# Optimization experiments

Measured on AMD Instinct MI355X. Metric: run time of the kernel, lower is better.

The kernel has to match this reference:

```python
import jax, jax.numpy as jnp
import numpy as np

L, B, T, V, E, H = 6, 4, 1024, 32000, 768, 12
D = E // H  # head_size = 64


def setup_inputs() -> dict:
    key = jax.random.key(0)
    ks = jax.random.split(key, 12)
    s = 0.02
    n = lambda k, shape: jax.random.normal(k, shape, jnp.float32) * s
    return {
        "idx": jax.random.randint(ks[0], (B, T), 0, V),
        "tok_emb": n(ks[1], (V, E)),
        "pos_emb": n(ks[2], (T, E)),
        "ln1_w": jnp.ones((L, E)), "ln1_b": jnp.zeros((L, E)),
        "wq": n(ks[3], (L, E, H, D)),
        "wk": n(ks[4], (L, E, H, D)),
        "wv": n(ks[5], (L, E, H, D)),
        "wo": n(ks[6], (L, E, E)), "bo": jnp.zeros((L, E)),
        "ln2_w": jnp.ones((L, E)), "ln2_b": jnp.zeros((L, E)),
        "w1": n(ks[7], (L, E, 4 * E)), "b1": jnp.zeros((L, 4 * E)),
        "w2": n(ks[8], (L, 4 * E, E)), "b2": jnp.zeros((L, E)),
        "lnf_w": jnp.ones((E,)), "lnf_b": jnp.zeros((E,)),
        "head_w": n(ks[9], (E, V)), "head_b": jnp.zeros((V,)),
    }


def _ln(x, w, b, eps=1e-5):
    m = x.mean(-1, keepdims=True)
    v = ((x - m) ** 2).mean(-1, keepdims=True)
    return (x - m) * jax.lax.rsqrt(v + eps) * w + b


def _forward(idx, tok_emb, pos_emb, ln1_w, ln1_b, wq, wk, wv, wo, bo,
             ln2_w, ln2_b, w1, b1, w2, b2, lnf_w, lnf_b, head_w, head_b):
    t = idx.shape[1]
    x = tok_emb[idx] + pos_emb[None, :t]          # [B,T,E]
    causal = jnp.tril(jnp.ones((t, t), bool))     # tril buffer
    scale = jnp.asarray(D, x.dtype) ** -0.5       # k.shape[-1] ** -0.5

    def block(x, p):
        l1w, l1b, Wq, Wk, Wv, Wo, Bo, l2w, l2b, W1, B1, W2, B2 = p
        h = _ln(x, l1w, l1b)
        q = jnp.einsum('btc,chd->bthd', h, Wq)
        k = jnp.einsum('btc,chd->bthd', h, Wk)
        v = jnp.einsum('btc,chd->bthd', h, Wv)
        wei = jnp.einsum('bqhd,bkhd->bhqk', q, k) * scale
        wei = jnp.where(causal, wei, -jnp.inf)
        wei = jax.nn.softmax(wei, axis=-1)
        att = jnp.einsum('bhqk,bkhd->bqhd', wei, v).reshape(x.shape)
        x = x + (att @ Wo + Bo)
        h2 = _ln(x, l2w, l2b)
        x = x + (jax.nn.relu(h2 @ W1 + B1) @ W2 + B2)
        return x, None

    params = (ln1_w, ln1_b, wq, wk, wv, wo, bo, ln2_w, ln2_b, w1, b1, w2, b2)
    x, _ = jax.lax.scan(block, x, params)
    x = _ln(x, lnf_w, lnf_b)
    return x @ head_w + head_b                    # [B,T,V] logits


def reference(idx, tok_emb, pos_emb, ln1_w, ln1_b, wq, wk, wv, wo, bo,
              ln2_w, ln2_b, w1, b1, w2, b2, lnf_w, lnf_b, head_w, head_b):
    return _forward(idx, tok_emb, pos_emb, ln1_w, ln1_b, wq, wk, wv, wo, bo,
                    ln2_w, ln2_b, w1, b1, w2, b2, lnf_w, lnf_b, head_w, head_b)
```

## Files before the change

### kernel.cpp

```cpp
#include <hip/hip_runtime.h>
#include <hip/hip_bf16.h>
#include <math.h>

#define L_LAYERS 6
#define BB 4
#define TT 1024
#define VV 32000
#define EE 768
#define HH 12
#define DD 64
#define BT (BB * TT)

typedef unsigned short u16;
typedef unsigned int   u32;
typedef __attribute__((ext_vector_type(8))) short short8;
typedef __attribute__((ext_vector_type(8))) unsigned short ushort8v;
typedef __attribute__((ext_vector_type(4))) float f32x4;

__device__ __forceinline__ float b2f_lo(u32 u) { union { u32 i; float f; } c; c.i = u << 16;          return c.f; }
__device__ __forceinline__ float b2f_hi(u32 u) { union { u32 i; float f; } c; c.i = u & 0xffff0000u;  return c.f; }
__device__ __forceinline__ u16  f2b(float f)   { union { float f; u32 i; } c{f}; u32 r = c.i + 0x7fffu + ((c.i >> 16) & 1u); return (u16)(r >> 16); }

__device__ __forceinline__ void gload16(const void* g, void* l) {
    __builtin_amdgcn_global_load_lds(
        (const __attribute__((address_space(1))) void*)g,
        (__attribute__((address_space(3))) void*)l, 16, 0, 0);
}

__global__ __launch_bounds__(256) void embed_kernel(
    const int* __restrict__ idx, const float* __restrict__ tok_emb,
    const float* __restrict__ pos_emb, float* __restrict__ x)
{
    int i = blockIdx.x * 256 + threadIdx.x;
    int e  = i % EE;
    int bt = i / EE;
    int t  = bt % TT;
    int tok = idx[bt];
    x[i] = tok_emb[(size_t)tok * EE + e] + pos_emb[(size_t)t * EE + e];
}

__global__ __launch_bounds__(256) void ln_kernel(
    const float* __restrict__ X, const float* __restrict__ w,
    const float* __restrict__ b, u16* __restrict__ Y)
{
    const int tid = threadIdx.x;
    const size_t row = blockIdx.x;
    const float* x = X + row * EE;

    float v0 = x[tid], v1 = x[tid + 256], v2 = x[tid + 512];

    __shared__ float red[256];
    red[tid] = v0 + v1 + v2;
    __syncthreads();
    for (int off = 128; off > 0; off >>= 1) {
        if (tid < off) red[tid] += red[tid + off];
        __syncthreads();
    }
    float mean = red[0] * (1.0f / EE);
    __syncthreads();
    float d0 = v0 - mean, d1 = v1 - mean, d2 = v2 - mean;
    red[tid] = d0 * d0 + d1 * d1 + d2 * d2;
    __syncthreads();
    for (int off = 128; off > 0; off >>= 1) {
        if (tid < off) red[tid] += red[tid + off];
        __syncthreads();
    }
    float rstd = rsqrtf(red[0] * (1.0f / EE) + 1e-5f);

    u16* y = Y + row * EE;
    y[tid]       = f2b(d0 * rstd * w[tid]       + b[tid]);
    y[tid + 256] = f2b(d1 * rstd * w[tid + 256] + b[tid + 256]);
    y[tid + 512] = f2b(d2 * rstd * w[tid + 512] + b[tid + 512]);
}

__device__ __forceinline__ void transpose_tile(
    const float* __restrict__ W, u16* __restrict__ Wt,
    int K, int N, int kt, int nt)
{
    __shared__ float t[32][33];
    const int k0 = kt * 32;
    const int n0 = nt * 32;
    const int c = threadIdx.x & 31;
    const int r = threadIdx.x >> 5;
    #pragma unroll
    for (int i = 0; i < 4; i++)
        t[r + i * 8][c] = W[(size_t)(k0 + r + i * 8) * N + n0 + c];
    __syncthreads();
    #pragma unroll
    for (int i = 0; i < 4; i++) {
        int rr = r + i * 8;
        Wt[(size_t)(n0 + rr) * K + k0 + c] = f2b(t[c][rr]);
    }
}

__global__ __launch_bounds__(256) void transpose_cvt(
    const float* __restrict__ W, u16* __restrict__ Wt, int K, int N)
{
    transpose_tile(W, Wt, K, N, blockIdx.y, blockIdx.x);
}

__global__ __launch_bounds__(256) void transpose_layer(
    const float* __restrict__ wq, const float* __restrict__ wk,
    const float* __restrict__ wv, const float* __restrict__ wo,
    const float* __restrict__ w1, const float* __restrict__ w2,
    u16* __restrict__ wt)
{
    const int t = blockIdx.x;
    if (t < 2304) {
        const int m = t / 576, r = t % 576;
        const float* Ws[4] = {wq, wk, wv, wo};
        transpose_tile(Ws[m], wt + (size_t)m * 768 * 768, 768, 768, r / 24, r % 24);
    } else if (t < 4608) {
        const int r = t - 2304;
        transpose_tile(w1, wt + (size_t)4 * 768 * 768, 768, 3072, r / 96, r % 96);
    } else {
        const int r = t - 4608;
        transpose_tile(w2, wt + (size_t)4 * 768 * 768 + (size_t)3072 * 768,
                       3072, 768, r / 24, r % 24);
    }
}

template<int RELU, int RES, int OUTBF, int MFRAG>
__global__ __launch_bounds__(256) void gemm_bf16(
    const u16* __restrict__ A, const u16* __restrict__ Bt,
    const float* __restrict__ bias, const float* __restrict__ res,
    void* __restrict__ Cv, int M, int N, int K)
{
    constexpr int TM = MFRAG * 32;
    __shared__ u16 As[TM * 64];
    __shared__ u16 Bs[128 * 64];

    const int tid  = threadIdx.x;
    const int lane = tid & 63;
    const int w    = tid >> 6;
    const int wr   = w >> 1, wc = w & 1;
    const int m0 = blockIdx.x * TM;
    const int n0 = blockIdx.y * 128;

    const int cs = (lane & 7) ^ (lane >> 3);
    const int rl = lane >> 3;

    int aoff[2 * MFRAG], boff[8];
    const int kq = lane >> 4;
    #pragma unroll
    for (int mi = 0; mi < MFRAG; mi++) {
        int rg = wr * (MFRAG * 16) + mi * 16 + (lane & 15);
        #pragma unroll
        for (int ks = 0; ks < 2; ks++)
            aoff[2 * mi + ks] = rg * 64 + (((ks * 4 + kq) ^ (rg & 7)) * 8);
    }
    #pragma unroll
    for (int ni = 0; ni < 4; ni++) {
        int rg = wc * 64 + ni * 16 + (lane & 15);
        #pragma unroll
        for (int ks = 0; ks < 2; ks++)
            boff[2 * ni + ks] = rg * 64 + (((ks * 4 + kq) ^ (rg & 7)) * 8);
    }

    f32x4 acc[MFRAG][4] = {};

    for (int k0 = 0; k0 < K; k0 += 64) {
        __syncthreads();
        #pragma unroll
        for (int i = 0; i < MFRAG; i++) {
            const int seg = i * 4 + w;
            const int row = seg * 8 + rl;
            gload16(A + (size_t)(m0 + row) * K + k0 + cs * 8, &As[seg * 512]);
        }
        #pragma unroll
        for (int i = 0; i < 4; i++) {
            const int seg = i * 4 + w;
            const int row = seg * 8 + rl;
            gload16(Bt + (size_t)(n0 + row) * K + k0 + cs * 8, &Bs[seg * 512]);
        }
        __syncthreads();
        #pragma unroll
        for (int ks = 0; ks < 2; ks++) {
            short8 af[MFRAG], bfv[4];
            #pragma unroll
            for (int mi = 0; mi < MFRAG; mi++) af[mi] = *(const short8*)&As[aoff[2 * mi + ks]];
            #pragma unroll
            for (int ni = 0; ni < 4; ni++) bfv[ni] = *(const short8*)&Bs[boff[2 * ni + ks]];
            #pragma unroll
            for (int mi = 0; mi < MFRAG; mi++)
                #pragma unroll
                for (int ni = 0; ni < 4; ni++)
                    acc[mi][ni] = __builtin_amdgcn_mfma_f32_16x16x32_bf16(
                        af[mi], bfv[ni], acc[mi][ni], 0, 0, 0);
        }
    }

    const int rbase = m0 + wr * (MFRAG * 16) + (lane >> 4) * 4;
    const int cbase = n0 + wc * 64 + (lane & 15);
    #pragma unroll
    for (int ni = 0; ni < 4; ni++) {
        const int c = cbase + ni * 16;
        const float bv = bias ? bias[c] : 0.0f;
        #pragma unroll
        for (int mi = 0; mi < MFRAG; mi++) {
            const int r = rbase + mi * 16;
            #pragma unroll
            for (int i = 0; i < 4; i++) {
                float v = acc[mi][ni][i] + bv;
                const size_t off = (size_t)(r + i) * N + c;
                if (RES)  v += res[off];
                if (RELU) v = fmaxf(v, 0.0f);
                if (OUTBF) ((u16*)Cv)[off] = f2b(v);
                else       ((float*)Cv)[off] = v;
            }
        }
    }
}

template<int RELU, int OUTBF>
__global__ __launch_bounds__(512, 2) void gemm256(
    const u16* __restrict__ A, const u16* __restrict__ Bt,
    const float* __restrict__ bias, void* __restrict__ Cv,
    int M, int N, int K)
{
    __shared__ u16 SA[2][256 * 64];
    __shared__ u16 SB[2][256 * 64];

    const int tid  = threadIdx.x;
    const int lane = tid & 63;
    const int w    = tid >> 6;
    const int wr   = w >> 2, wc = w & 3;

    const int gx  = gridDim.x;
    const int nwg = gx * gridDim.y;
    const int lin = blockIdx.y * gx + blockIdx.x;
    const int q8  = nwg >> 3;
    const int s   = (lin & 7) * q8 + (lin >> 3);
    const int m0  = (s % gx) * 256;
    const int n0  = (s / gx) * 256;

    const int cs = (lane & 7) ^ (lane >> 3);
    const int rl = lane >> 3;

    const int lr = lane & 15, kq = lane >> 4;
    int aoff[16], boff[8];
    #pragma unroll
    for (int mi = 0; mi < 8; mi++) {
        int rg = wr * 128 + mi * 16 + lr;
        #pragma unroll
        for (int ks = 0; ks < 2; ks++)
            aoff[2 * mi + ks] = rg * 64 + (((ks * 4 + kq) ^ (rg & 7)) * 8);
    }
    #pragma unroll
    for (int ni = 0; ni < 4; ni++) {
        int rg = wc * 64 + ni * 16 + lr;
        #pragma unroll
        for (int ks = 0; ks < 2; ks++)
            boff[2 * ni + ks] = rg * 64 + (((ks * 4 + kq) ^ (rg & 7)) * 8);
    }

    const int nt = K >> 6;

    auto STAGE = [&](int t, int bf) {
        const int k0 = t * 64;
        #pragma unroll
        for (int i = 0; i < 4; i++) {
            const int seg = i * 8 + w;
            const int row = seg * 8 + rl;
            gload16(A + (size_t)(m0 + row) * K + k0 + cs * 8, &SA[bf][seg * 512]);
        }
        #pragma unroll
        for (int i = 0; i < 4; i++) {
            const int seg = i * 8 + w;
            const int row = seg * 8 + rl;
            gload16(Bt + (size_t)(n0 + row) * K + k0 + cs * 8, &SB[bf][seg * 512]);
        }
    };

    f32x4 acc[8][4] = {};

    STAGE(0, 0);
    STAGE(1, 1);
    asm volatile("s_waitcnt vmcnt(8)" ::: "memory");
    __builtin_amdgcn_s_barrier();
    __builtin_amdgcn_sched_barrier(0);

    for (int t = 0; t < nt; t++) {
        const int cur = t & 1;
        __builtin_amdgcn_s_setprio(1);
        #pragma unroll
        for (int ks = 0; ks < 2; ks++) {
            short8 af[8], bv[4];
            #pragma unroll
            for (int mi = 0; mi < 8; mi++) af[mi] = *(const short8*)&SA[cur][aoff[2 * mi + ks]];
            #pragma unroll
            for (int ni = 0; ni < 4; ni++) bv[ni] = *(const short8*)&SB[cur][boff[2 * ni + ks]];
            #pragma unroll
            for (int mi = 0; mi < 8; mi++)
                #pragma unroll
                for (int ni = 0; ni < 4; ni++)
                    acc[mi][ni] = __builtin_amdgcn_mfma_f32_16x16x32_bf16(
                        af[mi], bv[ni], acc[mi][ni], 0, 0, 0);
        }
        __builtin_amdgcn_s_setprio(0);

        if (t < nt - 1) {
            __builtin_amdgcn_sched_barrier(0);
            __builtin_amdgcn_s_barrier();
            __builtin_amdgcn_sched_barrier(0);
            if (t + 2 < nt) {
                STAGE(t + 2, cur);
                asm volatile("s_waitcnt vmcnt(8)" ::: "memory");
            } else {
                asm volatile("s_waitcnt vmcnt(0)" ::: "memory");
            }
            __builtin_amdgcn_sched_barrier(0);
            __builtin_amdgcn_s_barrier();
            __builtin_amdgcn_sched_barrier(0);
        }
    }

    const int rbase = m0 + wr * 128 + (lane >> 4) * 4;
    const int cbase = n0 + wc * 64 + lr;
    #pragma unroll
    for (int ni = 0; ni < 4; ni++) {
        const int c = cbase + ni * 16;
        const float bvf = bias ? bias[c] : 0.0f;
        #pragma unroll
        for (int mi = 0; mi < 8; mi++) {
            const int r = rbase + mi * 16;
            #pragma unroll
            for (int i = 0; i < 4; i++) {
                float v = acc[mi][ni][i] + bvf;
                if (RELU) v = fmaxf(v, 0.0f);
                const size_t off = (size_t)(r + i) * N + c;
                if (OUTBF) ((u16*)Cv)[off] = f2b(v);
                else       ((float*)Cv)[off] = v;
            }
        }
    }
}

#define AST 76
__global__ __launch_bounds__(256) void attn_mfma(
    const u16* __restrict__ qkv, u16* __restrict__ O)
{
    const int tid = threadIdx.x;
    const int qi = blockIdx.x;
    const int h  = blockIdx.y;
    const int b  = blockIdx.z;
    const int q0 = qi * 64;

    __shared__ u16 Ks[64 * AST];
    __shared__ u16 Vt[64 * AST];
    __shared__ u16 Ps[64 * AST];

    const int lane = tid & 63;
    const int w    = tid >> 6;
    const int lr   = lane & 15;
    const int lk   = lane >> 4;

    const int sr = tid >> 2;
    const int sc = tid & 3;

    {
        const u16* src = qkv + (size_t)(b * TT + q0 + sr) * 2304 + h * 64 + sc * 16;
        *(ushort8v*)&Ps[sr * AST + sc * 16]     = *(const ushort8v*)src;
        *(ushort8v*)&Ps[sr * AST + sc * 16 + 8] = *(const ushort8v*)(src + 8);
    }
    __syncthreads();
    short8 aq[2];
    #pragma unroll
    for (int ks = 0; ks < 2; ks++)
        aq[ks] = *(const short8*)&Ps[(w * 16 + lr) * AST + lk * 8 + ks * 32];

    f32x4 oacc[4] = {};
    float m_run[4], l_run[4];
    #pragma unroll
    for (int i = 0; i < 4; i++) { m_run[i] = -3.0e38f; l_run[i] = 0.0f; }

    const int qrow = q0 + w * 16 + lk * 4;
    const int ntile = qi + 1;

    for (int t = 0; t < ntile; t++) {
        const int k0 = t * 64;
        __syncthreads();
        {
            const u16* ksrc = qkv + (size_t)(b * TT + k0 + sr) * 2304 + 768 + h * 64 + sc * 16;
            *(ushort8v*)&Ks[sr * AST + sc * 16]     = *(const ushort8v*)ksrc;
            *(ushort8v*)&Ks[sr * AST + sc * 16 + 8] = *(const ushort8v*)(ksrc + 8);
            const u16* vsrc = ksrc + 768;
            ushort8v v0 = *(const ushort8v*)vsrc;
            ushort8v v1 = *(const ushort8v*)(vsrc + 8);
            #pragma unroll
            for (int j = 0; j < 8; j++) Vt[(sc * 16 + j) * AST + sr]     = v0[j];
            #pragma unroll
            for (int j = 0; j < 8; j++) Vt[(sc * 16 + 8 + j) * AST + sr] = v1[j];
        }
        __syncthreads();

        f32x4 sfrag[4] = {};
        #pragma unroll
        for (int ks = 0; ks < 2; ks++)
            #pragma unroll
            for (int nt = 0; nt < 4; nt++) {
                short8 bk = *(const short8*)&Ks[(nt * 16 + lr) * AST + lk * 8 + ks * 32];
                sfrag[nt] = __builtin_amdgcn_mfma_f32_16x16x32_bf16(aq[ks], bk, sfrag[nt], 0, 0, 0);
            }

        float sv[4][4];
        #pragma unroll
        for (int i = 0; i < 4; i++) {
            float mx = -3.0e38f;
            #pragma unroll
            for (int nt = 0; nt < 4; nt++) {
                float s = sfrag[nt][i] * 0.125f;
                if (t == qi && (k0 + nt * 16 + lr) > (qrow + i)) s = -3.0e38f;
                sv[i][nt] = s;
                mx = fmaxf(mx, s);
            }
            mx = fmaxf(mx, __shfl_xor(mx, 1));
            mx = fmaxf(mx, __shfl_xor(mx, 2));
            mx = fmaxf(mx, __shfl_xor(mx, 4));
            mx = fmaxf(mx, __shfl_xor(mx, 8));
            const float m_new = fmaxf(m_run[i], mx);
            const float scale = __expf(m_run[i] - m_new);
            float rs = 0.0f;
            #pragma unroll
            for (int nt = 0; nt < 4; nt++) {
                float p = __expf(sv[i][nt] - m_new);
                sv[i][nt] = p;
                rs += p;
            }
            rs += __shfl_xor(rs, 1);
            rs += __shfl_xor(rs, 2);
            rs += __shfl_xor(rs, 4);
            rs += __shfl_xor(rs, 8);
            l_run[i] = l_run[i] * scale + rs;
            m_run[i] = m_new;
            #pragma unroll
            for (int dt = 0; dt < 4; dt++) oacc[dt][i] *= scale;
        }

        #pragma unroll
        for (int i = 0; i < 4; i++)
            #pragma unroll
            for (int nt = 0; nt < 4; nt++)
                Ps[(w * 16 + lk * 4 + i) * AST + nt * 16 + lr] = f2b(sv[i][nt]);
        __syncthreads();

        #pragma unroll
        for (int ks = 0; ks < 2; ks++) {
            short8 ap = *(const short8*)&Ps[(w * 16 + lr) * AST + lk * 8 + ks * 32];
            #pragma unroll
            for (int dt = 0; dt < 4; dt++) {
                short8 bv = *(const short8*)&Vt[(dt * 16 + lr) * AST + lk * 8 + ks * 32];
                oacc[dt] = __builtin_amdgcn_mfma_f32_16x16x32_bf16(ap, bv, oacc[dt], 0, 0, 0);
            }
        }
    }

    #pragma unroll
    for (int i = 0; i < 4; i++) {
        const float inv = 1.0f / l_run[i];
        u16* dst = O + (size_t)(b * TT + q0 + w * 16 + lk * 4 + i) * 768 + h * 64 + lr;
        #pragma unroll
        for (int dt = 0; dt < 4; dt++)
            dst[dt * 16] = f2b(oacc[dt][i] * inv);
    }
}

extern "C" void kernel_launch(void* const* d_in, const int* in_sizes, int n_in,
                              void* d_out, int out_size, void* d_ws, size_t ws_size,
                              hipStream_t stream)
{
    (void)in_sizes; (void)n_in; (void)out_size; (void)ws_size;

    const int*   idx     = (const int*)  d_in[0];
    const float* tok_emb = (const float*)d_in[1];
    const float* pos_emb = (const float*)d_in[2];
    const float* ln1_w   = (const float*)d_in[3];
    const float* ln1_b   = (const float*)d_in[4];
    const float* wq      = (const float*)d_in[5];
    const float* wk      = (const float*)d_in[6];
    const float* wv      = (const float*)d_in[7];
    const float* wo      = (const float*)d_in[8];
    const float* bo      = (const float*)d_in[9];
    const float* ln2_w   = (const float*)d_in[10];
    const float* ln2_b   = (const float*)d_in[11];
    const float* w1      = (const float*)d_in[12];
    const float* b1      = (const float*)d_in[13];
    const float* w2      = (const float*)d_in[14];
    const float* b2      = (const float*)d_in[15];
    const float* lnf_w   = (const float*)d_in[16];
    const float* lnf_b   = (const float*)d_in[17];
    const float* head_w  = (const float*)d_in[18];
    const float* head_b  = (const float*)d_in[19];
    float* out = (float*)d_out;

    const size_t S = (size_t)BT * EE;
    float* x   = (float*)d_ws;
    u16*  qkv  = (u16*)(x + S);
    u16*  hb   = qkv + (size_t)BT * 2304;
    u16*  ffh  = hb + S;
    u16*  wt   = ffh + (size_t)BT * 3072;

    embed_kernel<<<BT * EE / 256, 256, 0, stream>>>(idx, tok_emb, pos_emb, x);

    for (int l = 0; l < L_LAYERS; l++) {
        const size_t oE  = (size_t)l * EE;
        const size_t oEE = (size_t)l * EE * EE;
        const size_t oEF = (size_t)l * EE * 4 * EE;

        transpose_layer<<<6912, 256, 0, stream>>>(
            wq + oEE, wk + oEE, wv + oEE, wo + oEE, w1 + oEF, w2 + oEF, wt);

        ln_kernel<<<BT, 256, 0, stream>>>(x, ln1_w + oE, ln1_b + oE, hb);
        gemm256<0, 1><<<dim3(BT / 256, 2304 / 256), 512, 0, stream>>>(
            hb, wt, nullptr, qkv, BT, 2304, 768);
        attn_mfma<<<dim3(TT / 64, HH, BB), 256, 0, stream>>>(qkv, hb);
        gemm_bf16<0, 1, 0, 2><<<dim3(BT / 64, 768 / 128), 256, 0, stream>>>(
            hb, wt + (size_t)3 * 768 * 768, bo + oE, x, x, BT, 768, 768);
        ln_kernel<<<BT, 256, 0, stream>>>(x, ln2_w + oE, ln2_b + oE, hb);
        gemm256<1, 1><<<dim3(BT / 256, 3072 / 256), 512, 0, stream>>>(
            hb, wt + (size_t)4 * 768 * 768, b1 + (size_t)l * 4 * EE, ffh, BT, 3072, 768);
        gemm_bf16<0, 1, 0, 2><<<dim3(BT / 64, 768 / 128), 256, 0, stream>>>(
            ffh, wt + (size_t)4 * 768 * 768 + (size_t)3072 * 768, b2 + oE, x, x, BT, 768, 3072);
    }

    ln_kernel<<<BT, 256, 0, stream>>>(x, lnf_w, lnf_b, hb);
    transpose_cvt<<<dim3(VV / 32, EE / 32), 256, 0, stream>>>(head_w, wt, EE, VV);
    gemm256<0, 0><<<dim3(BT / 256, VV / 256), 512, 0, stream>>>(
        hb, wt, head_b, out, BT, VV, 768);
}
```

Baseline: 1.687 ms.

## Restructure 256x256 GEMM into eight-phase pipeline with half-tile staged loads

Replaces the double-buffered 256x256 GEMM main loop with a four-quadrant schedule. Each K-step is split into sub-phases that load half of the A/B fragments from LDS, issue the next tile's global-to-LDS loads in halves, and run the MFMA quadrants between barriers. Rows are permuted on load so each half-tile lands where the warps will read it. The aim is to overlap global loads, LDS reads and MFMA work more finely, at the cost of many more barriers per iteration and tricky buffer-reuse ordering.

```diff
diff --git a/kernel.cpp b/kernel.cpp
--- a/kernel.cpp
+++ b/kernel.cpp
@@ -213,7 +213,7 @@
 }
 
 template<int RELU, int OUTBF>
-__global__ __launch_bounds__(512, 2) void gemm256(
+__global__ __launch_bounds__(512, 2) void gemm8p(
     const u16* __restrict__ A, const u16* __restrict__ Bt,
     const float* __restrict__ bias, void* __restrict__ Cv,
     int M, int N, int K)
@@ -225,6 +225,8 @@
     const int lane = tid & 63;
     const int w    = tid >> 6;
     const int wr   = w >> 2, wc = w & 3;
+    const int lr   = lane & 15, kq = lane >> 4;
+    const int lr7  = lr & 7;
 
     const int gx  = gridDim.x;
     const int nwg = gx * gridDim.y;
@@ -237,95 +239,153 @@
     const int cs = (lane & 7) ^ (lane >> 3);
     const int rl = lane >> 3;
 
-    const int lr = lane & 15, kq = lane >> 4;
-    int aoff[16], boff[8];
-    #pragma unroll
-    for (int mi = 0; mi < 8; mi++) {
-        int rg = wr * 128 + mi * 16 + lr;
-        #pragma unroll
-        for (int ks = 0; ks < 2; ks++)
-            aoff[2 * mi + ks] = rg * 64 + (((ks * 4 + kq) ^ (rg & 7)) * 8);
-    }
-    #pragma unroll
-    for (int ni = 0; ni < 4; ni++) {
-        int rg = wc * 64 + ni * 16 + lr;
-        #pragma unroll
-        for (int ks = 0; ks < 2; ks++)
-            boff[2 * ni + ks] = rg * 64 + (((ks * 4 + kq) ^ (rg & 7)) * 8);
-    }
-
     const int nt = K >> 6;
 
-    auto STAGE = [&](int t, int bf) {
-        const int k0 = t * 64;
-        #pragma unroll
-        for (int i = 0; i < 4; i++) {
-            const int seg = i * 8 + w;
-            const int row = seg * 8 + rl;
-            gload16(A + (size_t)(m0 + row) * K + k0 + cs * 8, &SA[bf][seg * 512]);
-        }
-        #pragma unroll
-        for (int i = 0; i < 4; i++) {
-            const int seg = i * 8 + w;
-            const int row = seg * 8 + rl;
-            gload16(Bt + (size_t)(n0 + row) * K + k0 + cs * 8, &SB[bf][seg * 512]);
+    auto STAGE_A = [&](int tt, int h) {
+        u16* dst = &SA[tt & 1][0];
+        const int k0 = tt << 6;
+        #pragma unroll
+        for (int j = 0; j < 2; ++j) {
+            const int seg   = j * 8 + w;
+            const int rbase = h * 128 + seg * 8;
+            const int r     = rbase + rl;
+            const int grow  = (r & 63) | ((r & 128) >> 1) | ((r & 64) << 1);
+            gload16(A + (size_t)(m0 + grow) * K + k0 + cs * 8, dst + rbase * 64);
         }
     };
+    auto STAGE_B = [&](int tt, int h) {
+        u16* dst = &SB[tt & 1][0];
+        const int k0 = tt << 6;
+        #pragma unroll
+        for (int j = 0; j < 2; ++j) {
+            const int seg   = j * 8 + w;
+            const int rbase = h * 128 + seg * 8;
+            const int r     = rbase + rl;
+            const int grow  = (r & 31) | ((r & 96) << 1) | ((r & 128) >> 2);
+            gload16(Bt + (size_t)(n0 + grow) * K + k0 + cs * 8, dst + rbase * 64);
+        }
+    };
+
+    STAGE_A(0, 0); STAGE_A(0, 1); STAGE_B(0, 0); STAGE_B(0, 1);
+    STAGE_A(1, 0); STAGE_B(1, 0); STAGE_B(1, 1);
+    asm volatile("s_waitcnt vmcnt(6)" ::: "memory");
+    __builtin_amdgcn_s_barrier();
 
     f32x4 acc[8][4] = {};
 
-    STAGE(0, 0);
-    STAGE(1, 1);
-    asm volatile("s_waitcnt vmcnt(8)" ::: "memory");
-    __builtin_amdgcn_s_barrier();
-    __builtin_amdgcn_sched_barrier(0);
-
-    for (int t = 0; t < nt; t++) {
-        const int cur = t & 1;
+    for (int t = 0; t < nt; ++t) {
+        const int p = t & 1;
+        const u16* a0p = &SA[p][0] + wr * 4096 + lr * 64;
+        const u16* b0p = &SB[p][0] + wc * 2048 + lr * 64;
+        const int  c0  = (kq ^ lr7) * 8;
+        const int  c1  = ((4 + kq) ^ lr7) * 8;
+
+        short8 af[4][2], bf0[2][2], bf1[2][2];
+
+        #pragma unroll
+        for (int mi = 0; mi < 4; ++mi) {
+            af[mi][0] = *(const short8*)(a0p + mi * 1024 + c0);
+            af[mi][1] = *(const short8*)(a0p + mi * 1024 + c1);
+        }
+        #pragma unroll
+        for (int ni = 0; ni < 2; ++ni) {
+            bf0[ni][0] = *(const short8*)(b0p + ni * 1024 + c0);
+            bf0[ni][1] = *(const short8*)(b0p + ni * 1024 + c1);
+        }
+        if (t + 1 < nt) STAGE_A(t + 1, 1);
+        __builtin_amdgcn_sched_barrier(0);
+        __builtin_amdgcn_s_barrier();
+        asm volatile("s_waitcnt lgkmcnt(0)" ::: "memory");
+        __builtin_amdgcn_sched_barrier(0);
         __builtin_amdgcn_s_setprio(1);
         #pragma unroll
-        for (int ks = 0; ks < 2; ks++) {
-            short8 af[8], bv[4];
-            #pragma unroll
-            for (int mi = 0; mi < 8; mi++) af[mi] = *(const short8*)&SA[cur][aoff[2 * mi + ks]];
-            #pragma unroll
-            for (int ni = 0; ni < 4; ni++) bv[ni] = *(const short8*)&SB[cur][boff[2 * ni + ks]];
-            #pragma unroll
-            for (int mi = 0; mi < 8; mi++)
+        for (int ks = 0; ks < 2; ++ks)
+            #pragma unroll
+            for (int mi = 0; mi < 4; ++mi)
                 #pragma unroll
-                for (int ni = 0; ni < 4; ni++)
+                for (int ni = 0; ni < 2; ++ni)
                     acc[mi][ni] = __builtin_amdgcn_mfma_f32_16x16x32_bf16(
-                        af[mi], bv[ni], acc[mi][ni], 0, 0, 0);
-        }
+                        af[mi][ks], bf0[ni][ks], acc[mi][ni], 0, 0, 0);
         __builtin_amdgcn_s_setprio(0);
-
-        if (t < nt - 1) {
-            __builtin_amdgcn_sched_barrier(0);
-            __builtin_amdgcn_s_barrier();
-            __builtin_amdgcn_sched_barrier(0);
-            if (t + 2 < nt) {
-                STAGE(t + 2, cur);
-                asm volatile("s_waitcnt vmcnt(8)" ::: "memory");
-            } else {
-                asm volatile("s_waitcnt vmcnt(0)" ::: "memory");
-            }
-            __builtin_amdgcn_sched_barrier(0);
-            __builtin_amdgcn_s_barrier();
-            __builtin_amdgcn_sched_barrier(0);
-        }
-    }
-
-    const int rbase = m0 + wr * 128 + (lane >> 4) * 4;
+        __builtin_amdgcn_sched_barrier(0);
+        __builtin_amdgcn_s_barrier();
+
+        #pragma unroll
+        for (int ni = 0; ni < 2; ++ni) {
+            bf1[ni][0] = *(const short8*)(b0p + 8192 + ni * 1024 + c0);
+            bf1[ni][1] = *(const short8*)(b0p + 8192 + ni * 1024 + c1);
+        }
+        if (t + 2 < nt) STAGE_A(t + 2, 0);
+        __builtin_amdgcn_sched_barrier(0);
+        __builtin_amdgcn_s_barrier();
+        asm volatile("s_waitcnt lgkmcnt(0)" ::: "memory");
+        __builtin_amdgcn_sched_barrier(0);
+        __builtin_amdgcn_s_setprio(1);
+        #pragma unroll
+        for (int ks = 0; ks < 2; ++ks)
+            #pragma unroll
+            for (int mi = 0; mi < 4; ++mi)
+                #pragma unroll
+                for (int ni = 0; ni < 2; ++ni)
+                    acc[mi][2 + ni] = __builtin_amdgcn_mfma_f32_16x16x32_bf16(
+                        af[mi][ks], bf1[ni][ks], acc[mi][2 + ni], 0, 0, 0);
+        __builtin_amdgcn_s_setprio(0);
+        __builtin_amdgcn_sched_barrier(0);
+        __builtin_amdgcn_s_barrier();
+
+        #pragma unroll
+        for (int mi = 0; mi < 4; ++mi) {
+            af[mi][0] = *(const short8*)(a0p + 8192 + mi * 1024 + c0);
+            af[mi][1] = *(const short8*)(a0p + 8192 + mi * 1024 + c1);
+        }
+        if (t + 2 < nt) STAGE_B(t + 2, 0);
+        __builtin_amdgcn_sched_barrier(0);
+        __builtin_amdgcn_s_barrier();
+        asm volatile("s_waitcnt lgkmcnt(0)" ::: "memory");
+        __builtin_amdgcn_sched_barrier(0);
+        __builtin_amdgcn_s_setprio(1);
+        #pragma unroll
+        for (int ks = 0; ks < 2; ++ks)
+            #pragma unroll
+            for (int mi = 0; mi < 4; ++mi)
+                #pragma unroll
+                for (int ni = 0; ni < 2; ++ni)
+                    acc[4 + mi][ni] = __builtin_amdgcn_mfma_f32_16x16x32_bf16(
+                        af[mi][ks], bf0[ni][ks], acc[4 + mi][ni], 0, 0, 0);
+        __builtin_amdgcn_s_setprio(0);
+        __builtin_amdgcn_sched_barrier(0);
+        __builtin_amdgcn_s_barrier();
+
+        if (t + 2 < nt) STAGE_B(t + 2, 1);
+        __builtin_amdgcn_sched_barrier(0);
+        __builtin_amdgcn_s_barrier();
+        __builtin_amdgcn_s_setprio(1);
+        #pragma unroll
+        for (int ks = 0; ks < 2; ++ks)
+            #pragma unroll
+            for (int mi = 0; mi < 4; ++mi)
+                #pragma unroll
+                for (int ni = 0; ni < 2; ++ni)
+                    acc[4 + mi][2 + ni] = __builtin_amdgcn_mfma_f32_16x16x32_bf16(
+                        af[mi][ks], bf1[ni][ks], acc[4 + mi][2 + ni], 0, 0, 0);
+        __builtin_amdgcn_s_setprio(0);
+        if (t + 2 < nt)      { asm volatile("s_waitcnt vmcnt(6)" ::: "memory"); }
+        else if (t + 1 < nt) { asm volatile("s_waitcnt vmcnt(0)" ::: "memory"); }
+        __builtin_amdgcn_sched_barrier(0);
+        __builtin_amdgcn_s_barrier();
+    }
+
+    const int rbase = m0 + wr * 128 + kq * 4;
     const int cbase = n0 + wc * 64 + lr;
     #pragma unroll
-    for (int ni = 0; ni < 4; ni++) {
+    for (int ni = 0; ni < 4; ++ni) {
         const int c = cbase + ni * 16;
         const float bvf = bias ? bias[c] : 0.0f;
         #pragma unroll
-        for (int mi = 0; mi < 8; mi++) {
+        for (int mi = 0; mi < 8; ++mi) {
             const int r = rbase + mi * 16;
             #pragma unroll
-            for (int i = 0; i < 4; i++) {
+            for (int i = 0; i < 4; ++i) {
                 float v = acc[mi][ni][i] + bvf;
                 if (RELU) v = fmaxf(v, 0.0f);
                 const size_t off = (size_t)(r + i) * N + c;
@@ -511,13 +571,13 @@
             wq + oEE, wk + oEE, wv + oEE, wo + oEE, w1 + oEF, w2 + oEF, wt);
 
         ln_kernel<<<BT, 256, 0, stream>>>(x, ln1_w + oE, ln1_b + oE, hb);
-        gemm256<0, 1><<<dim3(BT / 256, 2304 / 256), 512, 0, stream>>>(
+        gemm8p<0, 1><<<dim3(BT / 256, 2304 / 256), 512, 0, stream>>>(
             hb, wt, nullptr, qkv, BT, 2304, 768);
         attn_mfma<<<dim3(TT / 64, HH, BB), 256, 0, stream>>>(qkv, hb);
         gemm_bf16<0, 1, 0, 2><<<dim3(BT / 64, 768 / 128), 256, 0, stream>>>(
             hb, wt + (size_t)3 * 768 * 768, bo + oE, x, x, BT, 768, 768);
         ln_kernel<<<BT, 256, 0, stream>>>(x, ln2_w + oE, ln2_b + oE, hb);
-        gemm256<1, 1><<<dim3(BT / 256, 3072 / 256), 512, 0, stream>>>(
+        gemm8p<1, 1><<<dim3(BT / 256, 3072 / 256), 512, 0, stream>>>(
             hb, wt + (size_t)4 * 768 * 768, b1 + (size_t)l * 4 * EE, ffh, BT, 3072, 768);
         gemm_bf16<0, 1, 0, 2><<<dim3(BT / 64, 768 / 128), 256, 0, stream>>>(
             ffh, wt + (size_t)4 * 768 * 768 + (size_t)3072 * 768, b2 + oE, x, x, BT, 768, 3072);
@@ -525,6 +585,6 @@
 
     ln_kernel<<<BT, 256, 0, stream>>>(x, lnf_w, lnf_b, hb);
     transpose_cvt<<<dim3(VV / 32, EE / 32), 256, 0, stream>>>(head_w, wt, EE, VV);
-    gemm256<0, 0><<<dim3(BT / 256, VV / 256), 512, 0, stream>>>(
+    gemm8p<0, 0><<<dim3(BT / 256, VV / 256), 512, 0, stream>>>(
         hb, wt, head_b, out, BT, VV, 768);
 }
```

Result: faster. 1.632 ms (-3.3%).
